# Kernel tuning notes

Measured on AMD Instinct MI355X. Metric: run time of the kernel, lower is better.

Reference implementation:

```python
import jax, jax.numpy as jnp
import numpy as np

SEQ_LEN = 4096
D_MODEL = 1024
OUT_DIM = 1024
KERNEL = 256
STRIDE = 16
NUM_HEADS = 16


def _p(key, *shape):
    return jax.random.normal(key, shape, dtype=jnp.float32) * 0.02


def setup_inputs() -> dict:
    key = jax.random.key(0)
    ks = jax.random.split(key, 12)
    return {
        "path": jax.random.normal(ks[0], (SEQ_LEN, D_MODEL), dtype=jnp.float32),
        # sliding_module (nn.MultiheadAttention, embed_dim=D_MODEL)
        "w_in1": _p(ks[1], 3 * D_MODEL, D_MODEL),
        "b_in1": jnp.zeros((3 * D_MODEL,), jnp.float32),
        "w_out1": _p(ks[2], D_MODEL, D_MODEL),
        "b_out1": jnp.zeros((D_MODEL,), jnp.float32),
        # linear_module
        "w_lin": _p(ks[3], OUT_DIM, D_MODEL),
        "b_lin": jnp.zeros((OUT_DIM,), jnp.float32),
        # accum_module (embed_dim=OUT_DIM)
        "w_in2": _p(ks[4], 3 * OUT_DIM, OUT_DIM),
        "b_in2": jnp.zeros((3 * OUT_DIM,), jnp.float32),
        "w_out2": _p(ks[5], OUT_DIM, OUT_DIM),
        "b_out2": jnp.zeros((OUT_DIM,), jnp.float32),
    }


def _mha(q, k, v, w_in, b_in, w_out, b_out, num_heads):
    """torch nn.MultiheadAttention math (dropout=0). q,k,v: [..., L, E]."""
    E = q.shape[-1]
    Dh = E // num_heads
    wq, wk, wv = jnp.split(w_in, 3, axis=0)
    bq, bk, bv = jnp.split(b_in, 3)
    def heads(t):
        return t.reshape(t.shape[:-1] + (num_heads, Dh))
    qh = heads(q @ wq.T + bq)
    kh = heads(k @ wk.T + bk)
    vh = heads(v @ wv.T + bv)
    scale = 1.0 / np.sqrt(Dh).astype(np.float32)
    att = jax.nn.softmax(jnp.einsum("...qhd,...khd->...hqk", qh, kh) * scale, axis=-1)
    out = jnp.einsum("...hqk,...khd->...qhd", att, vh)
    out = out.reshape(out.shape[:-2] + (E,))
    return out @ w_out.T + b_out


def reference(path, w_in1, b_in1, w_out1, b_out1, w_lin, b_lin,
              w_in2, b_in2, w_out2, b_out2):
    seq_len = path.shape[-2]
    slices_num = (seq_len - KERNEL) // STRIDE
    # overlapping windows: [slices_num, KERNEL, D_MODEL]
    idx = jnp.arange(slices_num)[:, None] * STRIDE + jnp.arange(KERNEL)[None, :]
    x = path[idx]
    # batched self-attention over windows
    x = _mha(x, x, x, w_in1, b_in1, w_out1, b_out1, NUM_HEADS)
    x = jax.nn.relu(x @ w_lin.T + b_lin)  # [slices_num, KERNEL, OUT_DIM]
    # sequential recurrent attention accumulation
    def step(cum_att, xi):
        new = _mha(xi, cum_att, cum_att, w_in2, b_in2, w_out2, b_out2, NUM_HEADS)
        return new, None
    cum_att, _ = jax.lax.scan(step, x[0], x[1:])
    return cum_att  # [KERNEL, OUT_DIM]
```

## Files before the change

kernel.cpp:

```cpp
#include <hip/hip_runtime.h>
#include <math.h>

#define D_MODEL 1024
#define N_WIN   240
#define TOK     256
#define NH      16
#define DH      64
#define CHUNK   8
#define NCHUNK  30
#define WIN     ((size_t)TOK * D_MODEL)

typedef unsigned short ushort_t;
typedef unsigned long long ull_t;
typedef __attribute__((ext_vector_type(8))) short short8;
typedef __attribute__((ext_vector_type(4))) float floatx4;

__device__ __forceinline__ ushort_t f2bf(float f) {
    unsigned u = __float_as_uint(f);
    unsigned lsb = (u >> 16) & 1u;
    u += 0x7fffu + lsb;
    return (ushort_t)(u >> 16);
}

__device__ __forceinline__ void st2_wt(ushort_t* p, ushort_t v) {
    unsigned vv = v;
    asm volatile("global_store_short %0, %1, off sc1"
                 :: "v"(p), "v"(vv) : "memory");
}
__device__ __forceinline__ void rel_drain() {
    asm volatile("s_waitcnt vmcnt(0)" ::: "memory");
}

#define GLDS(g, l) __builtin_amdgcn_global_load_lds( \
    (const __attribute__((address_space(1))) unsigned int*)(g), \
    (__attribute__((address_space(3))) unsigned int*)(l), 16, 0, 0)

__device__ __forceinline__ void grid_bar(unsigned* base, int g, unsigned s)
{
    rel_drain();
    __syncthreads();
    if (threadIdx.x == 0) {
        unsigned old = __hip_atomic_fetch_add(base + g * 32, 1u,
                __ATOMIC_RELAXED, __HIP_MEMORY_SCOPE_AGENT);
        if (old == 8u * s - 1u) {
            unsigned r = __hip_atomic_fetch_add(base + 256, 1u,
                    __ATOMIC_RELAXED, __HIP_MEMORY_SCOPE_AGENT);
            if (r == 8u * s - 1u)
                __hip_atomic_store(base + 288, s, __ATOMIC_RELAXED,
                                   __HIP_MEMORY_SCOPE_AGENT);
        }
        while (__hip_atomic_load(base + 288, __ATOMIC_RELAXED,
                                 __HIP_MEMORY_SCOPE_AGENT) < s)
            __builtin_amdgcn_s_sleep(1);
    }
    __syncthreads();
}

__device__ __forceinline__ void head_bar(unsigned* base, int h, unsigned s)
{
    rel_drain();
    __syncthreads();
    if (threadIdx.x == 0) {
        __hip_atomic_fetch_add(base + 384 + h * 32, 1u,
                __ATOMIC_RELAXED, __HIP_MEMORY_SCOPE_AGENT);
        while (__hip_atomic_load(base + 384 + h * 32, __ATOMIC_RELAXED,
                                 __HIP_MEMORY_SCOPE_AGENT) < 4u * s)
            __builtin_amdgcn_s_sleep(1);
    }
    __syncthreads();
}

__device__ __forceinline__ void help_bar(unsigned* base, int g, unsigned s)
{
    rel_drain();
    __syncthreads();
    if (threadIdx.x == 0) {
        unsigned old = __hip_atomic_fetch_add(base + 1024 + g * 32, 1u,
                __ATOMIC_RELAXED, __HIP_MEMORY_SCOPE_AGENT);
        if (old == 8u * s - 1u) {
            unsigned r = __hip_atomic_fetch_add(base + 1800, 1u,
                    __ATOMIC_RELAXED, __HIP_MEMORY_SCOPE_AGENT);
            if (r == 24u * s - 1u)
                __hip_atomic_store(base + 1832, s, __ATOMIC_RELAXED,
                                   __HIP_MEMORY_SCOPE_AGENT);
        }
        while (__hip_atomic_load(base + 1832, __ATOMIC_RELAXED,
                                 __HIP_MEMORY_SCOPE_AGENT) < s)
            __builtin_amdgcn_s_sleep(1);
    }
    __syncthreads();
}

__global__ __launch_bounds__(256) void cast_bf_k(
    const float* __restrict__ s, ushort_t* __restrict__ d, int n)
{
    int i = (blockIdx.x * 256 + threadIdx.x) * 4;
    if (i >= n) return;
    float4 v = *(const float4*)(s + i);
    ushort4 o;
    o.x = f2bf(v.x); o.y = f2bf(v.y); o.z = f2bf(v.z); o.w = f2bf(v.w);
    *(ushort4*)(d + i) = o;
}

__global__ __launch_bounds__(256) void transpose_k(
    const ushort_t* __restrict__ src, ushort_t* __restrict__ dst)
{
    __shared__ ushort_t t[64][65];
    const int bx = blockIdx.x * 64, by = blockIdx.y * 64;
    const int c = threadIdx.x & 63, r0 = threadIdx.x >> 6;
#pragma unroll
    for (int k = 0; k < 16; ++k) {
        int r = r0 + k * 4;
        t[r][c] = src[(size_t)(by + r) * 1024 + bx + c];
    }
    __syncthreads();
#pragma unroll
    for (int k = 0; k < 16; ++k) {
        int r = r0 + k * 4;
        dst[(size_t)(bx + r) * 1024 + by + c] = t[c][r];
    }
}

__global__ __launch_bounds__(256) void bc_k(
    const float* __restrict__ w_in2, const float* __restrict__ b_in2,
    const float* __restrict__ b_out2, float* __restrict__ bc)
{
    int n = blockIdx.x * 256 + threadIdx.x;
    const float* row = w_in2 + (size_t)(1024 + n) * 1024;
    float s = b_in2[1024 + n];
    for (int j = 0; j < 1024; j += 4) {
        float4 w = *(const float4*)(row + j);
        float4 b = *(const float4*)(b_out2 + j);
        s += w.x * b.x + w.y * b.y + w.z * b.z + w.w * b.w;
    }
    bc[n] = s;
}

template<bool GATHER, bool WT>
__device__ __forceinline__ void gemm_core(
    ushort_t* As, ushort_t* Bs,
    const ushort_t* __restrict__ A, int lda, int w0,
    const ushort_t* __restrict__ W, const float* __restrict__ bias,
    ushort_t* __restrict__ Cb, float* __restrict__ Cf, int ldc,
    int K, int m0, int n0, int co, int relu)
{
    const int tid = threadIdx.x;
    const int wave = tid >> 6, lane = tid & 63;
    const int wm = wave & 1, wn = wave >> 1;

    int r0 = m0 + (tid >> 2), r1 = r0 + 64;
    if (GATHER) {
        r0 = (w0 + (r0 >> 8)) * 16 + (r0 & 255);
        r1 = (w0 + (r1 >> 8)) * 16 + (r1 & 255);
    }
    const int kcol = (tid & 3) * 8;
    const ushort_t* gA0 = A + (size_t)r0 * lda + kcol;
    const ushort_t* gA1 = A + (size_t)r1 * lda + kcol;
    const ushort_t* pW  = W + (size_t)n0 * K;
    const ushort_t* gB0 = pW + (size_t)(tid >> 2) * K + kcol;
    const ushort_t* gB1 = gB0 + (size_t)64 * K;
    ushort_t* lA = As + wave * 512;
    ushort_t* lB = Bs + wave * 512;

    floatx4 acc[4][4];
#pragma unroll
    for (int i = 0; i < 4; ++i)
#pragma unroll
        for (int j = 0; j < 4; ++j) acc[i][j] = (floatx4){0.f, 0.f, 0.f, 0.f};

    const int fr = lane & 15, fk = (lane >> 4) * 8;
    const int arow = (wm * 64 + fr) * 32 + fk;
    const int brow = (wn * 64 + fr) * 32 + fk;

    for (int k0 = 0; k0 < K; k0 += 32) {
        GLDS(gA0 + k0, lA);
        GLDS(gA1 + k0, lA + 2048);
        GLDS(gB0 + k0, lB);
        GLDS(gB1 + k0, lB + 2048);
        __syncthreads();
        short8 a[4], b[4];
#pragma unroll
        for (int mi = 0; mi < 4; ++mi) a[mi] = *(const short8*)&As[arow + mi * 512];
#pragma unroll
        for (int ni = 0; ni < 4; ++ni) b[ni] = *(const short8*)&Bs[brow + ni * 512];
#pragma unroll
        for (int mi = 0; mi < 4; ++mi)
#pragma unroll
            for (int ni = 0; ni < 4; ++ni)
                acc[mi][ni] = __builtin_amdgcn_mfma_f32_16x16x32_bf16(
                    a[mi], b[ni], acc[mi][ni], 0, 0, 0);
        __syncthreads();
    }

    const int crq = (lane >> 4) * 4;
    const int ccol = lane & 15;
#pragma unroll
    for (int mi = 0; mi < 4; ++mi) {
#pragma unroll
        for (int ni = 0; ni < 4; ++ni) {
            int lc = wn * 64 + ni * 16 + ccol;
            float bz = bias[n0 + lc];
#pragma unroll
            for (int rg = 0; rg < 4; ++rg) {
                int row = m0 + wm * 64 + mi * 16 + crq + rg;
                float v = acc[mi][ni][rg] + bz;
                if (relu) v = fmaxf(v, 0.f);
                size_t off = (size_t)row * ldc + co + lc;
                if (Cb) {
                    if (WT) st2_wt(Cb + off, f2bf(v));
                    else    Cb[off] = f2bf(v);
                }
                if (Cf) Cf[off] = v;
            }
        }
    }
}

__global__ __launch_bounds__(256) void gemm_bf_k(
    const ushort_t* __restrict__ A, int lda,
    const ushort_t* __restrict__ W, const float* __restrict__ bias,
    ushort_t* __restrict__ Cb, float* __restrict__ Cf, int ldc,
    int K, int relu)
{
    __shared__ ushort_t As[128 * 32];
    __shared__ ushort_t Bs[128 * 32];
    gemm_core<false, false>(As, Bs, A, lda, 0, W, bias, Cb, Cf, ldc, K,
                            blockIdx.y * 128, blockIdx.x * 128, blockIdx.x * 128, relu);
}

__global__ __launch_bounds__(256) void gemm_qkv_k(
    const ushort_t* __restrict__ path_bf, const ushort_t* __restrict__ W,
    const float* __restrict__ bias, ushort_t* __restrict__ Cb, int w0)
{
    __shared__ ushort_t As[128 * 32];
    __shared__ ushort_t Bs[128 * 32];
    gemm_core<true, false>(As, Bs, path_bf, 1024, w0, W, bias, Cb, nullptr, 3072, 1024,
                           blockIdx.y * 128, blockIdx.x * 128, blockIdx.x * 128, 0);
}

#define PLD 260
#define VLD 132

struct AttnShared {
    ushort_t P[64 * PLD];
    ushort_t VT[64 * VLD];
    float    l[64];
};

__device__ void attn_body(AttnShared& sh,
    const ushort_t* __restrict__ qkv, ushort_t* __restrict__ ao,
    int rs, int h, int b)
{
    const ushort_t* base = qkv + (size_t)b * TOK * 3072;
    const ushort_t* Q = base;
    const ushort_t* K = base + 1024;
    const ushort_t* V = base + 2048;
    ushort_t* O = ao + (size_t)b * TOK * 1024;
    const int ldq = 3072, ldkv = 3072, ldo = 1024;
    const int tid = threadIdx.x;
    const int wave = tid >> 6, lane = tid & 63;
    const int fr = lane & 15, q = lane >> 4, fk = q * 8;
    const ushort_t* Qh = Q + (size_t)(rs * 64) * ldq + h * 64;
    const ushort_t* Kh = K + h * 64;
    const ushort_t* Vh = V + h * 64;
    const int m0 = wave * 16;

    floatx4 s[16];
#pragma unroll
    for (int nt = 0; nt < 16; ++nt) s[nt] = (floatx4){0.f, 0.f, 0.f, 0.f};
#pragma unroll
    for (int kc = 0; kc < 64; kc += 32) {
        short8 a = *(const short8*)(Qh + (size_t)(m0 + fr) * ldq + kc + fk);
#pragma unroll
        for (int nt = 0; nt < 16; ++nt) {
            short8 b2 = *(const short8*)(Kh + (size_t)(nt * 16 + fr) * ldkv + kc + fk);
            s[nt] = __builtin_amdgcn_mfma_f32_16x16x32_bf16(a, b2, s[nt], 0, 0, 0);
        }
    }

    float rmax[4] = {-INFINITY, -INFINITY, -INFINITY, -INFINITY};
#pragma unroll
    for (int nt = 0; nt < 16; ++nt)
#pragma unroll
        for (int rg = 0; rg < 4; ++rg) rmax[rg] = fmaxf(rmax[rg], s[nt][rg]);
#pragma unroll
    for (int d = 1; d < 16; d <<= 1)
#pragma unroll
        for (int rg = 0; rg < 4; ++rg)
            rmax[rg] = fmaxf(rmax[rg], __shfl_xor(rmax[rg], d));

    float rsum[4] = {0.f, 0.f, 0.f, 0.f};
#pragma unroll
    for (int nt = 0; nt < 16; ++nt) {
#pragma unroll
        for (int rg = 0; rg < 4; ++rg) {
            float p = __expf((s[nt][rg] - rmax[rg]) * 0.125f);
            rsum[rg] += p;
            sh.P[(m0 + q * 4 + rg) * PLD + nt * 16 + fr] = f2bf(p);
        }
    }
#pragma unroll
    for (int d = 1; d < 16; d <<= 1)
#pragma unroll
        for (int rg = 0; rg < 4; ++rg) rsum[rg] += __shfl_xor(rsum[rg], d);
    if (fr == 0) {
#pragma unroll
        for (int rg = 0; rg < 4; ++rg) sh.l[m0 + q * 4 + rg] = rsum[rg];
    }
    __syncthreads();

    floatx4 o[4];
#pragma unroll
    for (int i = 0; i < 4; ++i) o[i] = (floatx4){0.f, 0.f, 0.f, 0.f};

#pragma unroll
    for (int half = 0; half < 2; ++half) {
        {
            int r = tid & 127, cp = tid >> 7;
            const ushort_t* vrow = Vh + (size_t)(half * 128 + r) * ldkv + cp * 32;
#pragma unroll
            for (int c = 0; c < 4; ++c) {
                uint4 pk = *(const uint4*)(vrow + c * 8);
                int d0 = cp * 32 + c * 8;
                sh.VT[(d0 + 0) * VLD + r] = (ushort_t)(pk.x & 0xffff);
                sh.VT[(d0 + 1) * VLD + r] = (ushort_t)(pk.x >> 16);
                sh.VT[(d0 + 2) * VLD + r] = (ushort_t)(pk.y & 0xffff);
                sh.VT[(d0 + 3) * VLD + r] = (ushort_t)(pk.y >> 16);
                sh.VT[(d0 + 4) * VLD + r] = (ushort_t)(pk.z & 0xffff);
                sh.VT[(d0 + 5) * VLD + r] = (ushort_t)(pk.z >> 16);
                sh.VT[(d0 + 6) * VLD + r] = (ushort_t)(pk.w & 0xffff);
                sh.VT[(d0 + 7) * VLD + r] = (ushort_t)(pk.w >> 16);
            }
        }
        __syncthreads();
#pragma unroll
        for (int ks = 0; ks < 4; ++ks) {
            short8 a = *(const short8*)&sh.P[(m0 + fr) * PLD + half * 128 + ks * 32 + fk];
#pragma unroll
            for (int nt2 = 0; nt2 < 4; ++nt2) {
                short8 b2 = *(const short8*)&sh.VT[(nt2 * 16 + fr) * VLD + ks * 32 + fk];
                o[nt2] = __builtin_amdgcn_mfma_f32_16x16x32_bf16(a, b2, o[nt2], 0, 0, 0);
            }
        }
        __syncthreads();
    }

    float linv[4];
#pragma unroll
    for (int rg = 0; rg < 4; ++rg) linv[rg] = 1.f / sh.l[m0 + q * 4 + rg];
#pragma unroll
    for (int nt2 = 0; nt2 < 4; ++nt2)
#pragma unroll
        for (int rg = 0; rg < 4; ++rg) {
            int row = rs * 64 + m0 + q * 4 + rg;
            st2_wt(O + (size_t)row * ldo + h * 64 + nt2 * 16 + fr,
                   f2bf(o[nt2][rg] * linv[rg]));
        }
    __syncthreads();
}

__global__ __launch_bounds__(256) void attn_mfma_k(
    const ushort_t* __restrict__ qkv, ushort_t* __restrict__ ao)
{
    __shared__ AttnShared sh;
    attn_body(sh, qkv, ao, blockIdx.x, blockIdx.y, blockIdx.z);
}

#define KLD 76
#define TLD 264

struct ScanSmem {
    union {
        struct { ushort_t Ab[2][4096]; ushort_t Wb[2][8192]; } st;
        struct { ushort_t Kl[256 * KLD]; ushort_t Vt[64 * TLD];
                 ushort_t P[64 * TLD]; } at;
    };
};

__device__ __forceinline__ void stage_kv(
    const ushort_t* __restrict__ A64, const ushort_t* __restrict__ Wsel,
    int h, int k0, ushort_t* __restrict__ Ad, ushort_t* __restrict__ Wd,
    int wave, int lane)
{
#pragma unroll
    for (int t = 0; t < 2; ++t) {
        int j = wave * 128 + t * 64 + lane;
        int row = j >> 3;
        int blk = (j & 7) ^ (row & 7);
        GLDS(A64 + (size_t)row * 1024 + k0 + blk * 8,
             Ad + wave * 1024 + t * 512);
    }
#pragma unroll
    for (int t = 0; t < 4; ++t) {
        int j = wave * 256 + t * 64 + lane;
        int r = j >> 3;
        int blk = (j & 7) ^ (r & 7);
        int n = ((r >> 6) << 10) + h * 64 + (r & 63);
        GLDS(Wsel + (size_t)n * 1024 + k0 + blk * 8,
             Wd + wave * 2048 + t * 512);
    }
}

__device__ void scan_body(
    ScanSmem& sm, int h, int rs, int g,
    const ushort_t* __restrict__ Qchunk, int i0, int w0, int nsteps,
    const ushort_t* __restrict__ x0, ushort_t* __restrict__ AOb,
    ushort_t* __restrict__ KVx,
    const ushort_t* __restrict__ Wkv, const float* __restrict__ bkv,
    const ushort_t* __restrict__ Wc, const float* __restrict__ bc,
    unsigned* __restrict__ bar, unsigned s0)
{
    const int tid = threadIdx.x;
    const int wave = tid >> 6, lane = tid & 63;
    const int fr = lane & 15, q = lane >> 4, fk = q * 8;

    const int dbofs = (wave < 2 ? 0 : 1024) + h * 64 + (wave & 1) * 32;
    float bK1[2], bC1[2];
#pragma unroll
    for (int nt = 0; nt < 2; ++nt) {
        bK1[nt] = bkv[dbofs + nt * 16 + fr];
        bC1[nt] = bc[dbofs + nt * 16 + fr];
    }

    ushort_t* Kl = sm.at.Kl;
    ushort_t* Vt = sm.at.Vt;
    ushort_t* P  = sm.at.P;

    unsigned s = s0;
    for (int t0 = 0; t0 < nsteps; ++t0, ++s) {
        const int i = i0 + t0;
        const ushort_t* Asrc;
        const ushort_t* Wsel;
        if (i == 1) { Asrc = x0; Wsel = Wkv; }
        else {
            Asrc = AOb + (size_t)((i - 1) & 7) * WIN;
            Wsel = Wc;
        }
        const ushort_t* A64 = Asrc + (size_t)rs * 64 * 1024;
        ushort_t* KVs = KVx + (size_t)(i & 7) * (NH * 32768) + h * 32768;

        const int m0g = rs * 64 + wave * 16;
        const ushort_t* Qrow = Qchunk + (size_t)(i - w0) * WIN
            + (size_t)(m0g + fr) * 1024 + h * 64;
        short8 qf0 = *(const short8*)(Qrow);
        short8 qf1 = *(const short8*)(Qrow + 32);

        floatx4 acc[4][2];
#pragma unroll
        for (int mt = 0; mt < 4; ++mt)
#pragma unroll
            for (int nt = 0; nt < 2; ++nt)
                acc[mt][nt] = (floatx4){0.f, 0.f, 0.f, 0.f};

        stage_kv(A64, Wsel, h, 0, sm.st.Ab[0], sm.st.Wb[0], wave, lane);
#pragma unroll 1
        for (int t = 0; t < 16; ++t) {
            const int cur = t & 1;
            if (t < 15) {
                stage_kv(A64, Wsel, h, (t + 1) * 64,
                         sm.st.Ab[cur ^ 1], sm.st.Wb[cur ^ 1], wave, lane);
                asm volatile("s_waitcnt vmcnt(6)" ::: "memory");
            } else {
                asm volatile("s_waitcnt vmcnt(0)" ::: "memory");
            }
            __builtin_amdgcn_s_barrier();
            const ushort_t* Ac = sm.st.Ab[cur];
            const ushort_t* Wc_ = sm.st.Wb[cur];
#pragma unroll
            for (int kh = 0; kh < 2; ++kh) {
                const int pb = (((kh << 2) + q) ^ (fr & 7)) * 8;
                short8 a[4];
#pragma unroll
                for (int mt = 0; mt < 4; ++mt)
                    a[mt] = *(const short8*)&Ac[(mt * 16 + fr) * 64 + pb];
#pragma unroll
                for (int nt = 0; nt < 2; ++nt) {
                    short8 b = *(const short8*)
                        &Wc_[(wave * 32 + nt * 16 + fr) * 64 + pb];
#pragma unroll
                    for (int mt = 0; mt < 4; ++mt)
                        acc[mt][nt] = __builtin_amdgcn_mfma_f32_16x16x32_bf16(
                            a[mt], b, acc[mt][nt], 0, 0, 0);
                }
            }
            asm volatile("s_waitcnt lgkmcnt(0)" ::: "memory");
            __builtin_amdgcn_sched_barrier(0);
            __builtin_amdgcn_s_barrier();
        }

        {
            ushort_t* Kx = KVs;
            ushort_t* Vx = KVs + 16384;
#pragma unroll
            for (int mt = 0; mt < 4; ++mt) {
#pragma unroll
                for (int nt = 0; nt < 2; ++nt) {
                    const float bz = (i == 1) ? bK1[nt] : bC1[nt];
                    const int d = (wave & 1) * 32 + nt * 16 + fr;
#pragma unroll
                    for (int rg = 0; rg < 4; ++rg) {
                        const int key = rs * 64 + mt * 16 + q * 4 + rg;
                        const float v = acc[mt][nt][rg] + bz;
                        if (wave < 2) st2_wt(Kx + key * 64 + d, f2bf(v));
                        else          st2_wt(Vx + d * 256 + key, f2bf(v));
                    }
                }
            }
        }
        head_bar(bar, h, s);

        {
            const ushort_t* Kx = KVs;
            const ushort_t* Vx = KVs + 16384;
            uint4 kb4[8], vb4[8];
            const ushort_t* kr = Kx + tid * 64;
            const int vd = tid >> 2, vq = tid & 3;
            const ushort_t* vr = Vx + vd * 256 + vq * 64;
#pragma unroll
            for (int s8 = 0; s8 < 8; ++s8)
                kb4[s8] = *(const uint4*)(kr + s8 * 8);
#pragma unroll
            for (int s8 = 0; s8 < 8; ++s8)
                vb4[s8] = *(const uint4*)(vr + s8 * 8);
            const int kp = (tid >> 4) & 3;
#pragma unroll
            for (int s8 = 0; s8 < 8; ++s8) {
                int ks = (s8 + kp) & 7;
                *(uint4*)&Kl[tid * KLD + ks * 8] = kb4[ks];
            }
            const int vp = vq << 1;
#pragma unroll
            for (int s8 = 0; s8 < 8; ++s8) {
                int vs = (s8 + vp) & 7;
                *(uint4*)&Vt[vd * TLD + vq * 64 + vs * 8] = vb4[vs];
            }
        }
        __syncthreads();

        ushort_t* AOcur = AOb + (size_t)(i & 7) * WIN;
        {
            const int pl0 = wave * 16;
            floatx4 sc[16];
#pragma unroll
            for (int nt = 0; nt < 16; ++nt) sc[nt] = (floatx4){0.f, 0.f, 0.f, 0.f};
#pragma unroll
            for (int kc = 0; kc < 64; kc += 32) {
                short8 a = (kc == 0) ? qf0 : qf1;
#pragma unroll
                for (int nt = 0; nt < 16; ++nt) {
                    short8 b = *(const short8*)&Kl[(nt * 16 + fr) * KLD + kc + fk];
                    sc[nt] = __builtin_amdgcn_mfma_f32_16x16x32_bf16(
                        a, b, sc[nt], 0, 0, 0);
                }
            }
            float rmax[4] = {-INFINITY, -INFINITY, -INFINITY, -INFINITY};
#pragma unroll
            for (int nt = 0; nt < 16; ++nt)
#pragma unroll
                for (int rg = 0; rg < 4; ++rg) rmax[rg] = fmaxf(rmax[rg], sc[nt][rg]);
#pragma unroll
            for (int d = 1; d < 16; d <<= 1)
#pragma unroll
                for (int rg = 0; rg < 4; ++rg)
                    rmax[rg] = fmaxf(rmax[rg], __shfl_xor(rmax[rg], d));
            float rsum[4] = {0.f, 0.f, 0.f, 0.f};
#pragma unroll
            for (int nt = 0; nt < 16; ++nt) {
#pragma unroll
                for (int rg = 0; rg < 4; ++rg) {
                    float p = __expf((sc[nt][rg] - rmax[rg]) * 0.125f);
                    rsum[rg] += p;
                    P[(pl0 + q * 4 + rg) * TLD + nt * 16 + fr] = f2bf(p);
                }
            }
#pragma unroll
            for (int d = 1; d < 16; d <<= 1)
#pragma unroll
                for (int rg = 0; rg < 4; ++rg) rsum[rg] += __shfl_xor(rsum[rg], d);

            floatx4 o[4];
#pragma unroll
            for (int nt = 0; nt < 4; ++nt) o[nt] = (floatx4){0.f, 0.f, 0.f, 0.f};
#pragma unroll
            for (int kt = 0; kt < 8; ++kt) {
                short8 a = *(const short8*)&P[(pl0 + fr) * TLD + kt * 32 + fk];
#pragma unroll
                for (int nt = 0; nt < 4; ++nt) {
                    short8 b = *(const short8*)&Vt[(nt * 16 + fr) * TLD + kt * 32 + fk];
                    o[nt] = __builtin_amdgcn_mfma_f32_16x16x32_bf16(
                        a, b, o[nt], 0, 0, 0);
                }
            }
            float linv[4];
#pragma unroll
            for (int rg = 0; rg < 4; ++rg) linv[rg] = 1.f / rsum[rg];
#pragma unroll
            for (int nt = 0; nt < 4; ++nt)
#pragma unroll
                for (int rg = 0; rg < 4; ++rg) {
                    int row = m0g + q * 4 + rg;
                    st2_wt(AOcur + (size_t)row * 1024 + h * 64 + nt * 16 + fr,
                           f2bf(o[nt][rg] * linv[rg]));
                }
        }
        grid_bar(bar, g, s);
    }
}

struct GemmSmem { ushort_t As[128 * 32]; ushort_t Bs[128 * 32]; };
union FusedSmem { ScanSmem scan; GemmSmem gem; AttnShared att; };

__global__ __launch_bounds__(256, 1) void fused_k(
    const ushort_t* __restrict__ Qchunk, int i0, int w0, int nsteps,
    const ushort_t* __restrict__ x0, ushort_t* __restrict__ AOb,
    ushort_t* __restrict__ KVx,
    const ushort_t* __restrict__ Wkv, const float* __restrict__ bkv,
    const ushort_t* __restrict__ Wc, const float* __restrict__ bc,
    unsigned* __restrict__ bar, unsigned s0,
    int do_help, int w0n,
    const ushort_t* __restrict__ path_bf,
    const ushort_t* __restrict__ w_in1, const float* __restrict__ b_in1,
    ushort_t* __restrict__ qkv, ushort_t* __restrict__ ao,
    ushort_t* __restrict__ ybuf,
    const ushort_t* __restrict__ w_out1, const float* __restrict__ b_out1,
    const ushort_t* __restrict__ w_lin, const float* __restrict__ b_lin,
    ushort_t* __restrict__ Xc,
    const ushort_t* __restrict__ w_in2, const float* __restrict__ b_in2,
    ushort_t* __restrict__ Qnext, unsigned hs0)
{
    __shared__ FusedSmem sm;
    const int wg = blockIdx.x;
    const int x = wg & 7, y = wg >> 3;

    if (x < 2) {
        const int scanIdx = x * 32 + y;
        const int h  = (x << 3) | (y >> 2);
        const int rs = y & 3;
        const int g  = scanIdx & 7;
        scan_body(sm.scan, h, rs, g,
                  Qchunk, i0, w0, nsteps, x0, AOb, KVx,
                  Wkv, bkv, Wc, bc, bar, s0);
        return;
    }
    if (!do_help) return;

    const int hw = (x - 2) * 32 + y;
    const int hg = hw >> 3;

    for (int t = hw; t < 384; t += 192) {
        int bx = t % 24, by = t / 24;
        gemm_core<true, true>(sm.gem.As, sm.gem.Bs, path_bf, 1024, w0n,
                              w_in1, b_in1, qkv, nullptr, 3072, 1024,
                              by * 128, bx * 128, bx * 128, 0);
    }
    help_bar(bar, hg, hs0);

    for (int t = hw; t < 512; t += 192) {
        int rs = t & 3, h = (t >> 2) & 15, b = t >> 6;
        attn_body(sm.att, qkv, ao, rs, h, b);
    }
    help_bar(bar, hg, hs0 + 1);

    for (int t = hw; t < 128; t += 192) {
        int bx = t & 7, by = t >> 3;
        gemm_core<false, true>(sm.gem.As, sm.gem.Bs, ao, 1024, 0,
                               w_out1, b_out1, ybuf, nullptr, 1024, 1024,
                               by * 128, bx * 128, bx * 128, 0);
    }
    help_bar(bar, hg, hs0 + 2);

    for (int t = hw; t < 128; t += 192) {
        int bx = t & 7, by = t >> 3;
        gemm_core<false, true>(sm.gem.As, sm.gem.Bs, ybuf, 1024, 0,
                               w_lin, b_lin, Xc, nullptr, 1024, 1024,
                               by * 128, bx * 128, bx * 128, 1);
    }
    help_bar(bar, hg, hs0 + 3);

    for (int t = hw; t < 128; t += 192) {
        int bx = t & 7, by = t >> 3;
        gemm_core<false, true>(sm.gem.As, sm.gem.Bs, Xc, 1024, 0,
                               w_in2, b_in2, Qnext, nullptr, 1024, 1024,
                               by * 128, bx * 128, bx * 128, 0);
    }
}

extern "C" void kernel_launch(void* const* d_in, const int* in_sizes, int n_in,
                              void* d_out, int out_size, void* d_ws, size_t ws_size,
                              hipStream_t stream)
{
    const float* path   = (const float*)d_in[0];
    const float* w_in1  = (const float*)d_in[1];
    const float* b_in1  = (const float*)d_in[2];
    const float* w_out1 = (const float*)d_in[3];
    const float* b_out1 = (const float*)d_in[4];
    const float* w_lin  = (const float*)d_in[5];
    const float* b_lin  = (const float*)d_in[6];
    const float* w_in2  = (const float*)d_in[7];
    const float* b_in2  = (const float*)d_in[8];
    const float* w_out2 = (const float*)d_in[9];
    const float* b_out2 = (const float*)d_in[10];
    float* out = (float*)d_out;

    unsigned* bar = (unsigned*)d_ws;
    float* bc      = (float*)d_ws + 2048;
    float* zerosf  = bc + 2048;
    ushort_t* ws = (ushort_t*)d_ws + 16384;
    ushort_t* path_bf  = ws;
    ushort_t* w_in1_bf = path_bf  + (size_t)4096 * 1024;
    ushort_t* w_out1_bf= w_in1_bf + (size_t)3072 * 1024;
    ushort_t* w_lin_bf = w_out1_bf+ (size_t)1024 * 1024;
    ushort_t* w_in2_bf = w_lin_bf + (size_t)1024 * 1024;
    ushort_t* w_out2_bf= w_in2_bf + (size_t)3072 * 1024;
    ushort_t* WoT_bf   = w_out2_bf+ (size_t)1024 * 1024;
    ushort_t* Wc_bf    = WoT_bf   + (size_t)1024 * 1024;
    ushort_t* qkv_bf   = Wc_bf    + (size_t)2048 * 1024;
    ushort_t* ao_bf    = qkv_bf   + (size_t)2048 * 3072;
    ushort_t* ybuf_bf  = ao_bf    + (size_t)2048 * 1024;
    ushort_t* Xbuf     = ybuf_bf  + (size_t)2048 * 1024;
    ushort_t* Qb0      = Xbuf     + (size_t)2048 * 1024;
    ushort_t* Qb1      = Qb0      + (size_t)2048 * 1024;
    ushort_t* AOb      = Qb1      + (size_t)2048 * 1024;
    ushort_t* x0buf    = AOb + 8 * WIN;
    ushort_t* dummy    = x0buf + WIN;
    ushort_t* KVx      = dummy + WIN;
    ushort_t* Qb[2] = {Qb0, Qb1};

    hipMemsetAsync(bar, 0, 8192, stream);
    hipMemsetAsync(zerosf, 0, 1024 * sizeof(float), stream);

    cast_bf_k<<<4096, 256, 0, stream>>>(path,  path_bf,  4096 * 1024);
    cast_bf_k<<<3072, 256, 0, stream>>>(w_in1, w_in1_bf, 3072 * 1024);
    cast_bf_k<<<1024, 256, 0, stream>>>(w_out1, w_out1_bf, 1024 * 1024);
    cast_bf_k<<<1024, 256, 0, stream>>>(w_lin, w_lin_bf, 1024 * 1024);
    cast_bf_k<<<3072, 256, 0, stream>>>(w_in2, w_in2_bf, 3072 * 1024);
    cast_bf_k<<<1024, 256, 0, stream>>>(w_out2, w_out2_bf, 1024 * 1024);

    transpose_k<<<dim3(16, 16), 256, 0, stream>>>(w_out2_bf, WoT_bf);
    bc_k<<<8, 256, 0, stream>>>(w_in2, b_in2, b_out2, bc);
    gemm_bf_k<<<dim3(8, 16), 256, 0, stream>>>(
        w_in2_bf + (size_t)1024 * 1024, 1024, WoT_bf, zerosf,
        Wc_bf, nullptr, 1024, 1024, 0);

    gemm_qkv_k<<<dim3(24, 16), 256, 0, stream>>>(
        path_bf, w_in1_bf, b_in1, qkv_bf, 0);
    attn_mfma_k<<<dim3(4, NH, CHUNK), 256, 0, stream>>>(qkv_bf, ao_bf);
    gemm_bf_k<<<dim3(8, 16), 256, 0, stream>>>(
        ao_bf, 1024, w_out1_bf, b_out1, ybuf_bf, nullptr, 1024, 1024, 0);
    gemm_bf_k<<<dim3(8, 16), 256, 0, stream>>>(
        ybuf_bf, 1024, w_lin_bf, b_lin, Xbuf, nullptr, 1024, 1024, 1);
    gemm_bf_k<<<dim3(8, 16), 256, 0, stream>>>(
        Xbuf, 1024, w_in2_bf, b_in2, Qb[0], nullptr, 1024, 1024, 0);
    hipMemcpyAsync(x0buf, Xbuf, WIN * sizeof(ushort_t),
                   hipMemcpyDeviceToDevice, stream);

    unsigned sbase = 1;
    for (int c = 0; c < NCHUNK; ++c) {
        int w0 = c * CHUNK;
        int i0 = (c == 0) ? 1 : w0;
        int nsteps = (c == 0) ? CHUNK - 1 : CHUNK;
        int do_help = (c + 1 < NCHUNK) ? 1 : 0;
        int w0n = (c + 1) * CHUNK;
        unsigned hs0 = (unsigned)(c * 4 + 1);
        const ushort_t* Qcur = Qb[c & 1];
        ushort_t* Qnext = Qb[(c + 1) & 1];
        const ushort_t* x0P = x0buf;
        ushort_t* AObP = AOb;
        ushort_t* KVxP = KVx;
        const ushort_t* WkvP = w_in2_bf + (size_t)1024 * 1024;
        const float* bkvP = b_in2 + 1024;
        const ushort_t* WcP = Wc_bf;
        const float* bcP = bc;
        unsigned* barP = bar;
        unsigned sb = sbase;
        const ushort_t* pathP = path_bf;
        const ushort_t* win1P = w_in1_bf;
        const float* bin1P = b_in1;
        ushort_t* qkvP = qkv_bf;
        ushort_t* aoP = ao_bf;
        ushort_t* ybufP = ybuf_bf;
        const ushort_t* wout1P = w_out1_bf;
        const float* bout1P = b_out1;
        const ushort_t* wlinP = w_lin_bf;
        const float* blinP = b_lin;
        ushort_t* XP = Xbuf;
        const ushort_t* win2P = w_in2_bf;
        const float* bin2P = b_in2;
        void* args[] = {&Qcur, &i0, &w0, &nsteps, &x0P, &AObP, &KVxP,
                        &WkvP, &bkvP, &WcP, &bcP, &barP, &sb,
                        &do_help, &w0n, &pathP, &win1P, &bin1P,
                        &qkvP, &aoP, &ybufP, &wout1P, &bout1P,
                        &wlinP, &blinP, &XP, &win2P, &bin2P, &Qnext, &hs0};
        hipLaunchCooperativeKernel((void*)fused_k, dim3(256), dim3(256),
                                   args, 0, stream);
        sbase += (unsigned)nsteps;
    }

    gemm_bf_k<<<dim3(8, 2), 256, 0, stream>>>(
        AOb + (size_t)((N_WIN - 1) & 7) * WIN, 1024, w_out2_bf, b_out2,
        dummy, out, 1024, 1024, 0);
}
```

Before: 6.972 ms.

## Overlap scan barriers with weight prefetch and local K/V LDS writes

Splits K/V staging into separate A and W loads, with W triple-buffered and prefetched two k-tiles ahead. The head and grid barriers are split into arrive and wait phases so that the next step's weights and Q fragments are prefetched while waiting. Each block writes its own K/V slice straight into LDS and only reads the other blocks' slices from global memory. V is stored with packed 8-byte writes. This targets barrier stalls and redundant global traffic in the serial recurrent scan, at the cost of more LDS (a third W buffer) and more complex vmcnt accounting.

```diff
diff --git a/kernel.cpp b/kernel.cpp
--- a/kernel.cpp
+++ b/kernel.cpp
@@ -26,6 +26,12 @@
     unsigned vv = v;
     asm volatile("global_store_short %0, %1, off sc1"
                  :: "v"(p), "v"(vv) : "memory");
+}
+__device__ __forceinline__ void st8_wt(ushort_t* p, ushort4 v) {
+    ull_t dv = (ull_t)((unsigned)v.x | ((unsigned)v.y << 16))
+             | ((ull_t)((unsigned)v.z | ((unsigned)v.w << 16)) << 32);
+    asm volatile("global_store_dwordx2 %0, %1, off sc1"
+                 :: "v"(p), "v"(dv) : "memory");
 }
 __device__ __forceinline__ void rel_drain() {
     asm volatile("s_waitcnt vmcnt(0)" ::: "memory");
@@ -51,20 +57,6 @@
         }
         while (__hip_atomic_load(base + 288, __ATOMIC_RELAXED,
                                  __HIP_MEMORY_SCOPE_AGENT) < s)
-            __builtin_amdgcn_s_sleep(1);
-    }
-    __syncthreads();
-}
-
-__device__ __forceinline__ void head_bar(unsigned* base, int h, unsigned s)
-{
-    rel_drain();
-    __syncthreads();
-    if (threadIdx.x == 0) {
-        __hip_atomic_fetch_add(base + 384 + h * 32, 1u,
-                __ATOMIC_RELAXED, __HIP_MEMORY_SCOPE_AGENT);
-        while (__hip_atomic_load(base + 384 + h * 32, __ATOMIC_RELAXED,
-                                 __HIP_MEMORY_SCOPE_AGENT) < 4u * s)
             __builtin_amdgcn_s_sleep(1);
     }
     __syncthreads();
@@ -371,15 +363,14 @@
 
 struct ScanSmem {
     union {
-        struct { ushort_t Ab[2][4096]; ushort_t Wb[2][8192]; } st;
+        struct { ushort_t Ab[2][4096]; ushort_t Wb[3][8192]; } st;
         struct { ushort_t Kl[256 * KLD]; ushort_t Vt[64 * TLD];
                  ushort_t P[64 * TLD]; } at;
     };
 };
 
-__device__ __forceinline__ void stage_kv(
-    const ushort_t* __restrict__ A64, const ushort_t* __restrict__ Wsel,
-    int h, int k0, ushort_t* __restrict__ Ad, ushort_t* __restrict__ Wd,
+__device__ __forceinline__ void stage_A(
+    const ushort_t* __restrict__ A64, int k0, ushort_t* __restrict__ Ad,
     int wave, int lane)
 {
 #pragma unroll
@@ -390,6 +381,12 @@
         GLDS(A64 + (size_t)row * 1024 + k0 + blk * 8,
              Ad + wave * 1024 + t * 512);
     }
+}
+
+__device__ __forceinline__ void stage_W(
+    const ushort_t* __restrict__ Wsel, int h, int k0,
+    ushort_t* __restrict__ Wd, int wave, int lane)
+{
 #pragma unroll
     for (int t = 0; t < 4; ++t) {
         int j = wave * 256 + t * 64 + lane;
@@ -413,6 +410,7 @@
     const int tid = threadIdx.x;
     const int wave = tid >> 6, lane = tid & 63;
     const int fr = lane & 15, q = lane >> 4, fk = q * 8;
+    const int m0g = rs * 64 + wave * 16;
 
     const int dbofs = (wave < 2 ? 0 : 1024) + h * 64 + (wave & 1) * 32;
     float bK1[2], bC1[2];
@@ -426,25 +424,30 @@
     ushort_t* Vt = sm.at.Vt;
     ushort_t* P  = sm.at.P;
 
+    short8 qf0, qf1;
+    {
+        const int i = i0;
+        const ushort_t* Wsel0 = (i == 1) ? Wkv : Wc;
+        stage_W(Wsel0, h, 0,  sm.st.Wb[0], wave, lane);
+        stage_W(Wsel0, h, 64, sm.st.Wb[1], wave, lane);
+        const ushort_t* Qrow = Qchunk + (size_t)(i - w0) * WIN
+            + (size_t)(m0g + fr) * 1024 + h * 64;
+        qf0 = *(const short8*)(Qrow);
+        qf1 = *(const short8*)(Qrow + 32);
+        const ushort_t* Asrc0 = (i == 1) ? x0
+            : AOb + (size_t)((i - 1) & 7) * WIN;
+        stage_A(Asrc0 + (size_t)rs * 64 * 1024, 0, sm.st.Ab[0], wave, lane);
+    }
+
     unsigned s = s0;
     for (int t0 = 0; t0 < nsteps; ++t0, ++s) {
         const int i = i0 + t0;
-        const ushort_t* Asrc;
-        const ushort_t* Wsel;
-        if (i == 1) { Asrc = x0; Wsel = Wkv; }
-        else {
-            Asrc = AOb + (size_t)((i - 1) & 7) * WIN;
-            Wsel = Wc;
-        }
+        const ushort_t* Asrc = (i == 1) ? x0
+            : AOb + (size_t)((i - 1) & 7) * WIN;
+        const ushort_t* Wsel = (i == 1) ? Wkv : Wc;
         const ushort_t* A64 = Asrc + (size_t)rs * 64 * 1024;
         ushort_t* KVs = KVx + (size_t)(i & 7) * (NH * 32768) + h * 32768;
 
-        const int m0g = rs * 64 + wave * 16;
-        const ushort_t* Qrow = Qchunk + (size_t)(i - w0) * WIN
-            + (size_t)(m0g + fr) * 1024 + h * 64;
-        short8 qf0 = *(const short8*)(Qrow);
-        short8 qf1 = *(const short8*)(Qrow + 32);
-
         floatx4 acc[4][2];
 #pragma unroll
         for (int mt = 0; mt < 4; ++mt)
@@ -452,20 +455,21 @@
             for (int nt = 0; nt < 2; ++nt)
                 acc[mt][nt] = (floatx4){0.f, 0.f, 0.f, 0.f};
 
-        stage_kv(A64, Wsel, h, 0, sm.st.Ab[0], sm.st.Wb[0], wave, lane);
 #pragma unroll 1
         for (int t = 0; t < 16; ++t) {
-            const int cur = t & 1;
-            if (t < 15) {
-                stage_kv(A64, Wsel, h, (t + 1) * 64,
-                         sm.st.Ab[cur ^ 1], sm.st.Wb[cur ^ 1], wave, lane);
+            if (t < 15)
+                stage_A(A64, (t + 1) * 64, sm.st.Ab[(t + 1) & 1], wave, lane);
+            if (t < 14)
+                stage_W(Wsel, h, (t + 2) * 64, sm.st.Wb[(t + 2) % 3], wave, lane);
+            if (t == 15)
+                asm volatile("s_waitcnt vmcnt(0)" ::: "memory");
+            else if (t == 0 || t == 14)
                 asm volatile("s_waitcnt vmcnt(6)" ::: "memory");
-            } else {
-                asm volatile("s_waitcnt vmcnt(0)" ::: "memory");
-            }
+            else
+                asm volatile("s_waitcnt vmcnt(10)" ::: "memory");
             __builtin_amdgcn_s_barrier();
-            const ushort_t* Ac = sm.st.Ab[cur];
-            const ushort_t* Wc_ = sm.st.Wb[cur];
+            const ushort_t* Ac  = sm.st.Ab[t & 1];
+            const ushort_t* Wc_ = sm.st.Wb[t % 3];
 #pragma unroll
             for (int kh = 0; kh < 2; ++kh) {
                 const int pb = (((kh << 2) + q) ^ (fr & 7)) * 8;
@@ -488,51 +492,92 @@
             __builtin_amdgcn_s_barrier();
         }
 
-        {
-            ushort_t* Kx = KVs;
-            ushort_t* Vx = KVs + 16384;
-#pragma unroll
-            for (int mt = 0; mt < 4; ++mt) {
-#pragma unroll
-                for (int nt = 0; nt < 2; ++nt) {
-                    const float bz = (i == 1) ? bK1[nt] : bC1[nt];
-                    const int d = (wave & 1) * 32 + nt * 16 + fr;
+        ushort_t* Kx = KVs;
+        ushort_t* Vx = KVs + 16384;
+#pragma unroll
+        for (int mt = 0; mt < 4; ++mt) {
+#pragma unroll
+            for (int nt = 0; nt < 2; ++nt) {
+                const float bz = (i == 1) ? bK1[nt] : bC1[nt];
+                const int d = (wave & 1) * 32 + nt * 16 + fr;
+                if (wave < 2) {
 #pragma unroll
                     for (int rg = 0; rg < 4; ++rg) {
                         const int key = rs * 64 + mt * 16 + q * 4 + rg;
-                        const float v = acc[mt][nt][rg] + bz;
-                        if (wave < 2) st2_wt(Kx + key * 64 + d, f2bf(v));
-                        else          st2_wt(Vx + d * 256 + key, f2bf(v));
+                        st2_wt(Kx + key * 64 + d, f2bf(acc[mt][nt][rg] + bz));
                     }
-                }
-            }
-        }
-        head_bar(bar, h, s);
+                } else {
+                    ushort4 pv;
+                    pv.x = f2bf(acc[mt][nt][0] + bz);
+                    pv.y = f2bf(acc[mt][nt][1] + bz);
+                    pv.z = f2bf(acc[mt][nt][2] + bz);
+                    pv.w = f2bf(acc[mt][nt][3] + bz);
+                    st8_wt(Vx + d * 256 + rs * 64 + mt * 16 + q * 4, pv);
+                }
+            }
+        }
+        rel_drain();
+        __syncthreads();
+        if (tid == 0)
+            __hip_atomic_fetch_add(bar + 384 + h * 32, 1u,
+                    __ATOMIC_RELAXED, __HIP_MEMORY_SCOPE_AGENT);
+
+#pragma unroll
+        for (int mt = 0; mt < 4; ++mt) {
+#pragma unroll
+            for (int nt = 0; nt < 2; ++nt) {
+                const float bz = (i == 1) ? bK1[nt] : bC1[nt];
+                const int d = (wave & 1) * 32 + nt * 16 + fr;
+                if (wave < 2) {
+#pragma unroll
+                    for (int rg = 0; rg < 4; ++rg) {
+                        const int key = rs * 64 + mt * 16 + q * 4 + rg;
+                        Kl[key * KLD + d] = f2bf(acc[mt][nt][rg] + bz);
+                    }
+                } else {
+                    ushort4 pv;
+                    pv.x = f2bf(acc[mt][nt][0] + bz);
+                    pv.y = f2bf(acc[mt][nt][1] + bz);
+                    pv.z = f2bf(acc[mt][nt][2] + bz);
+                    pv.w = f2bf(acc[mt][nt][3] + bz);
+                    *(ushort4*)&Vt[d * TLD + rs * 64 + mt * 16 + q * 4] = pv;
+                }
+            }
+        }
+        if (tid == 0) {
+            while (__hip_atomic_load(bar + 384 + h * 32, __ATOMIC_RELAXED,
+                                     __HIP_MEMORY_SCOPE_AGENT) < 4u * s)
+                __builtin_amdgcn_s_sleep(1);
+        }
+        __syncthreads();
 
         {
-            const ushort_t* Kx = KVs;
-            const ushort_t* Vx = KVs + 16384;
-            uint4 kb4[8], vb4[8];
-            const ushort_t* kr = Kx + tid * 64;
+            if (wave != rs) {
+                const ushort_t* kr = Kx + tid * 64;
+                uint4 kb4[8];
+#pragma unroll
+                for (int s8 = 0; s8 < 8; ++s8)
+                    kb4[s8] = *(const uint4*)(kr + s8 * 8);
+                const int kp = (tid >> 4) & 3;
+#pragma unroll
+                for (int s8 = 0; s8 < 8; ++s8) {
+                    int ks = (s8 + kp) & 7;
+                    *(uint4*)&Kl[tid * KLD + ks * 8] = kb4[ks];
+                }
+            }
             const int vd = tid >> 2, vq = tid & 3;
-            const ushort_t* vr = Vx + vd * 256 + vq * 64;
-#pragma unroll
-            for (int s8 = 0; s8 < 8; ++s8)
-                kb4[s8] = *(const uint4*)(kr + s8 * 8);
-#pragma unroll
-            for (int s8 = 0; s8 < 8; ++s8)
-                vb4[s8] = *(const uint4*)(vr + s8 * 8);
-            const int kp = (tid >> 4) & 3;
-#pragma unroll
-            for (int s8 = 0; s8 < 8; ++s8) {
-                int ks = (s8 + kp) & 7;
-                *(uint4*)&Kl[tid * KLD + ks * 8] = kb4[ks];
-            }
-            const int vp = vq << 1;
-#pragma unroll
-            for (int s8 = 0; s8 < 8; ++s8) {
-                int vs = (s8 + vp) & 7;
-                *(uint4*)&Vt[vd * TLD + vq * 64 + vs * 8] = vb4[vs];
+            if (vq != rs) {
+                const ushort_t* vr = Vx + vd * 256 + vq * 64;
+                uint4 vb4[8];
+#pragma unroll
+                for (int s8 = 0; s8 < 8; ++s8)
+                    vb4[s8] = *(const uint4*)(vr + s8 * 8);
+                const int vp = vq << 1;
+#pragma unroll
+                for (int s8 = 0; s8 < 8; ++s8) {
+                    int vs = (s8 + vp) & 7;
+                    *(uint4*)&Vt[vd * TLD + vq * 64 + vs * 8] = vb4[vs];
+                }
             }
         }
         __syncthreads();
@@ -603,7 +648,38 @@
                            f2bf(o[nt][rg] * linv[rg]));
                 }
         }
-        grid_bar(bar, g, s);
+
+        rel_drain();
+        __syncthreads();
+        if (tid == 0) {
+            unsigned old = __hip_atomic_fetch_add(bar + g * 32, 1u,
+                    __ATOMIC_RELAXED, __HIP_MEMORY_SCOPE_AGENT);
+            if (old == 8u * s - 1u) {
+                unsigned r = __hip_atomic_fetch_add(bar + 256, 1u,
+                        __ATOMIC_RELAXED, __HIP_MEMORY_SCOPE_AGENT);
+                if (r == 8u * s - 1u)
+                    __hip_atomic_store(bar + 288, s, __ATOMIC_RELAXED,
+                                       __HIP_MEMORY_SCOPE_AGENT);
+            }
+        }
+        const bool more = (t0 + 1 < nsteps);
+        if (more) {
+            stage_W(Wc, h, 0,  sm.st.Wb[0], wave, lane);
+            stage_W(Wc, h, 64, sm.st.Wb[1], wave, lane);
+            const ushort_t* Qrow = Qchunk + (size_t)(i + 1 - w0) * WIN
+                + (size_t)(m0g + fr) * 1024 + h * 64;
+            qf0 = *(const short8*)(Qrow);
+            qf1 = *(const short8*)(Qrow + 32);
+        }
+        if (tid == 0) {
+            while (__hip_atomic_load(bar + 288, __ATOMIC_RELAXED,
+                                     __HIP_MEMORY_SCOPE_AGENT) < s)
+                __builtin_amdgcn_s_sleep(1);
+        }
+        __syncthreads();
+        if (more)
+            stage_A(AOb + (size_t)(i & 7) * WIN + (size_t)rs * 64 * 1024, 0,
+                    sm.st.Ab[0], wave, lane);
     }
 }
 
@@ -751,8 +827,8 @@
         ybuf_bf, 1024, w_lin_bf, b_lin, Xbuf, nullptr, 1024, 1024, 1);
     gemm_bf_k<<<dim3(8, 16), 256, 0, stream>>>(
         Xbuf, 1024, w_in2_bf, b_in2, Qb[0], nullptr, 1024, 1024, 0);
-    hipMemcpyAsync(x0buf, Xbuf, WIN * sizeof(ushort_t),
-                   hipMemcpyDeviceToDevice, stream);
+    (void)hipMemcpyAsync(x0buf, Xbuf, WIN * sizeof(ushort_t),
+                         hipMemcpyDeviceToDevice, stream);
 
     unsigned sbase = 1;
     for (int c = 0; c < NCHUNK; ++c) {
```

Result: faster. 6.434 ms (-7.7%).
